# Performance work log

Measured on AMD Instinct MI355X. Metric: run time of the kernel, lower is better.

Reference implementation:

```python
import jax, jax.numpy as jnp
import numpy as np

B, IN, OUT = 8192, 1024, 1024
GRID_SIZE, SPLINE_ORDER = 5, 3
GRID_LO, GRID_HI = -1.0, 1.0
LN_EPS = 1e-5


def make_grid():
    h = (GRID_HI - GRID_LO) / GRID_SIZE
    g = jnp.linspace(GRID_LO - h * SPLINE_ORDER, GRID_HI + h * SPLINE_ORDER,
                     GRID_SIZE + 2 * SPLINE_ORDER + 1, dtype=jnp.float32)
    return jnp.broadcast_to(g, (IN, g.shape[0]))  # [IN, 12]


def setup_inputs() -> dict:
    key = jax.random.key(0)
    k1, k2, k3 = jax.random.split(key, 3)
    # kaiming_uniform_ linear: bound = sqrt(3/fan_in)
    bw_bound = float(np.sqrt(3.0 / IN))
    sw_bound = float(np.sqrt(3.0 / (IN * 8)))
    return {
        "x": jax.random.normal(k1, (B, IN), dtype=jnp.float32),
        "base_weight": jax.random.uniform(k2, (OUT, IN), minval=-bw_bound, maxval=bw_bound, dtype=jnp.float32),
        "spline_weight": jax.random.uniform(k3, (OUT, IN, GRID_SIZE + SPLINE_ORDER), minval=-sw_bound, maxval=sw_bound, dtype=jnp.float32),
        "grid": make_grid(),
        "ln_gamma": jnp.ones((OUT,), dtype=jnp.float32),
        "ln_beta": jnp.zeros((OUT,), dtype=jnp.float32),
        "prelu_a": jnp.full((1,), 0.25, dtype=jnp.float32),
    }


def _bspline_bases(x, grid):
    # x: [B, IN]; grid: [IN, 12] -> bases: [B, IN, GRID_SIZE+SPLINE_ORDER]
    xu = x[:, :, None]                      # [B, IN, 1]
    g = grid[None, :, :]                    # [1, IN, 12]
    bases = ((xu >= g[..., :-1]) & (xu < g[..., 1:])).astype(x.dtype)
    for k in range(1, SPLINE_ORDER + 1):
        left = g[..., :-(k + 1)]
        right = g[..., k:-1]
        g_rshift = g[..., k + 1:]
        g_lshift = g[..., 1:-k]
        dr = right - left
        dd = g_rshift - g_lshift
        dr = jnp.where(dr == 0, jnp.ones_like(dr), dr)
        dd = jnp.where(dd == 0, jnp.ones_like(dd), dd)
        bases = (xu - left) / dr * bases[..., :-1] + (g_rshift - xu) / dd * bases[..., 1:]
    return bases


def reference(x, base_weight, spline_weight, grid, ln_gamma, ln_beta, prelu_a):
    base_out = jnp.dot(jax.nn.gelu(x, approximate=False), base_weight.T)  # [B, OUT]
    bases = _bspline_bases(x, grid)                                        # [B, IN, 8]
    spline_out = jnp.einsum('bik,oik->bo', bases, spline_weight)           # [B, OUT]
    y = base_out + spline_out
    mu = jnp.mean(y, axis=-1, keepdims=True)
    var = jnp.mean(jnp.square(y - mu), axis=-1, keepdims=True)
    yn = (y - mu) * jax.lax.rsqrt(var + LN_EPS) * ln_gamma + ln_beta
    return jnp.where(yn >= 0, yn, prelu_a * yn)
```

## Files before the change

### kernel.cpp

```cpp
#include <hip/hip_runtime.h>
#include <hip/hip_bf16.h>

typedef __attribute__((ext_vector_type(8))) short bf16x8;
typedef __attribute__((ext_vector_type(4))) float f32x4;

#define KTOT 9216
#define KHALF 4608
#define NB   8192
#define NIN  1024
#define NOUT 1024

__device__ __forceinline__ void load_lds16(const void* g, void* l) {
  __builtin_amdgcn_global_load_lds(
      (const __attribute__((address_space(1))) void*)g,
      (__attribute__((address_space(3))) void*)l, 16, 0, 0);
}

__global__ void prep(const float* __restrict__ x,
                     const float* __restrict__ grid,
                     __hip_bfloat16* __restrict__ A,
                     const float* __restrict__ bw,
                     const float* __restrict__ sw,
                     __hip_bfloat16* __restrict__ W) {
  if (blockIdx.x < 4096) {
    const int tid = blockIdx.x * blockDim.x + threadIdx.x;
    const int i  = tid & (NIN - 1);
    const int b0 = (tid >> 10) << 3;

    float g[12];
#pragma unroll
    for (int j = 0; j < 12; ++j) g[j] = grid[j];

    float invdr1[10], invdd1[10], invdr2[9], invdd2[9], invdr3[8], invdd3[8];
#pragma unroll
    for (int j = 0; j < 10; ++j) {
      invdr1[j] = __builtin_amdgcn_rcpf(g[j + 1] - g[j]);
      invdd1[j] = __builtin_amdgcn_rcpf(g[j + 2] - g[j + 1]);
    }
#pragma unroll
    for (int j = 0; j < 9; ++j) {
      invdr2[j] = __builtin_amdgcn_rcpf(g[j + 2] - g[j]);
      invdd2[j] = __builtin_amdgcn_rcpf(g[j + 3] - g[j + 1]);
    }
#pragma unroll
    for (int j = 0; j < 8; ++j) {
      invdr3[j] = __builtin_amdgcn_rcpf(g[j + 3] - g[j]);
      invdd3[j] = __builtin_amdgcn_rcpf(g[j + 4] - g[j + 1]);
    }

    for (int bb = 0; bb < 8; ++bb) {
      const int b = b0 + bb;
      const float xv = x[(size_t)b * NIN + i];
      const float ge = 0.5f * xv * (1.0f + erff(xv * 0.70710678118654752f));
      __hip_bfloat16* Arow = A + (size_t)b * KTOT;
      Arow[i] = __float2bfloat16(ge);

      float bas[11];
#pragma unroll
      for (int j = 0; j < 11; ++j)
        bas[j] = (xv >= g[j] && xv < g[j + 1]) ? 1.0f : 0.0f;
#pragma unroll
      for (int j = 0; j < 10; ++j)
        bas[j] = (xv - g[j]) * invdr1[j] * bas[j] + (g[j + 2] - xv) * invdd1[j] * bas[j + 1];
#pragma unroll
      for (int j = 0; j < 9; ++j)
        bas[j] = (xv - g[j]) * invdr2[j] * bas[j] + (g[j + 3] - xv) * invdd2[j] * bas[j + 1];
#pragma unroll
      for (int j = 0; j < 8; ++j)
        bas[j] = (xv - g[j]) * invdr3[j] * bas[j] + (g[j + 4] - xv) * invdd3[j] * bas[j + 1];

      union { __hip_bfloat16 h[8]; uint4 v; } u;
#pragma unroll
      for (int k = 0; k < 8; ++k) u.h[k] = __float2bfloat16(bas[k]);
      *reinterpret_cast<uint4*>(Arow + NIN + i * 8) = u.v;
    }
  } else {
    const int idx = (blockIdx.x - 4096) * blockDim.x + threadIdx.x;
    const int o  = idx / 1152;
    const int c8 = (idx - o * 1152) * 8;
    const float* src = (c8 < 1024) ? (bw + (size_t)o * 1024 + c8)
                                   : (sw + (size_t)o * 8192 + (c8 - 1024));
    float4 f0 = reinterpret_cast<const float4*>(src)[0];
    float4 f1 = reinterpret_cast<const float4*>(src)[1];
    union { __hip_bfloat16 h[8]; uint4 v; } u;
    u.h[0] = __float2bfloat16(f0.x); u.h[1] = __float2bfloat16(f0.y);
    u.h[2] = __float2bfloat16(f0.z); u.h[3] = __float2bfloat16(f0.w);
    u.h[4] = __float2bfloat16(f1.x); u.h[5] = __float2bfloat16(f1.y);
    u.h[6] = __float2bfloat16(f1.z); u.h[7] = __float2bfloat16(f1.w);
    *reinterpret_cast<uint4*>(W + (size_t)o * KTOT + c8) = u.v;
  }
}

__global__ __launch_bounds__(512, 2)
void gemm_2b(const __hip_bfloat16* __restrict__ A,
             const __hip_bfloat16* __restrict__ Bw,
             float* __restrict__ P0,
             float* __restrict__ P1w) {
  extern __shared__ char smem[];

  const int tid  = threadIdx.x;
  const int lane = tid & 63;
  const int wave = tid >> 6;
  const int wr = wave >> 2;
  const int wc = wave & 3;

  const int orig = blockIdx.x;
  const int bid  = (orig & 7) * 32 + (orig >> 3);
  const int ks    = bid & 1;
  const int tileN = (bid >> 1) & 3;
  const int tileM = bid >> 3;
  const size_t brow = (size_t)tileM * 256;
  const size_t bcol = (size_t)tileN * 256;
  const int kbeg = ks * KHALF;

  const __hip_bfloat16* Ab = A  + brow * KTOT;
  const __hip_bfloat16* Bb = Bw + bcol * KTOT;
  float* C = ks ? P1w : P0;

  const int swsrc = ((tid & 7) ^ ((tid >> 3) & 7)) * 8;
  const __hip_bfloat16* srcA = Ab + (size_t)(tid >> 3) * KTOT + kbeg + swsrc;
  const __hip_bfloat16* srcB = Bb + (size_t)(tid >> 3) * KTOT + kbeg + swsrc;
  const int wdst = wave * 1024;

#define AB_(buf)  (smem + (buf) * 32768)
#define BB_(slot) (smem + 98304 + (slot) * 32768)

  auto stageA = [&](int buf, int h, int kt) {
    const __hip_bfloat16* g = srcA + (size_t)h * (128 * KTOT) + (size_t)kt * 64;
    char* d = AB_(buf) + h * 16384 + wdst;
    load_lds16(g, d);
    load_lds16(g + (size_t)64 * KTOT, d + 8192);
  };
  auto stageB = [&](int slot, int h, int kt) {
    const __hip_bfloat16* g = srcB + (size_t)h * (128 * KTOT) + (size_t)kt * 64;
    char* d = BB_(slot) + h * 16384 + wdst;
    load_lds16(g, d);
    load_lds16(g + (size_t)64 * KTOT, d + 8192);
  };

  const int fr = lane & 15;
  const int hi = lane >> 4;
  const int sw = (fr & 7) << 4;
  const int ax0 = (hi * 16) ^ sw;
  const int ax1 = (64 + hi * 16) ^ sw;

  bf16x8 a[4][2], b[4][2];
  f32x4 acc[8][4] = {};

#define RD_A(BUF, MH) { \
    const char* Ah = AB_(BUF) + wr * 16384 + (MH) * 8192; \
    _Pragma("unroll") \
    for (int mi2 = 0; mi2 < 4; ++mi2) { \
      const char* p = Ah + (mi2 * 16 + fr) * 128; \
      a[mi2][0] = *(const bf16x8*)(p + ax0); \
      a[mi2][1] = *(const bf16x8*)(p + ax1); } }

#define RD_B(SLOT, NH) { \
    const char* Bh = BB_(SLOT) + (wc >> 1) * 16384 + ((wc & 1) * 64 + (NH) * 32) * 128; \
    _Pragma("unroll") \
    for (int ni2 = 0; ni2 < 2; ++ni2) { \
      const char* p = Bh + (ni2 * 16 + fr) * 128; \
      b[(NH) * 2 + ni2][0] = *(const bf16x8*)(p + ax0); \
      b[(NH) * 2 + ni2][1] = *(const bf16x8*)(p + ax1); } }

#define PH_SYNC() do { \
    asm volatile("" ::: "memory"); \
    __builtin_amdgcn_s_barrier(); \
    asm volatile("s_waitcnt lgkmcnt(0)" ::: "memory"); \
    __builtin_amdgcn_sched_barrier(0); } while (0)

#define QMFMA(MH, NH) do { \
    __builtin_amdgcn_s_setprio(1); \
    _Pragma("unroll") \
    for (int mi2 = 0; mi2 < 4; ++mi2) \
      _Pragma("unroll") \
      for (int ni2 = 0; ni2 < 2; ++ni2) \
        _Pragma("unroll") \
        for (int kk = 0; kk < 2; ++kk) \
          acc[(MH) * 4 + mi2][(NH) * 2 + ni2] = \
            __builtin_amdgcn_mfma_f32_16x16x32_bf16(a[mi2][kk], b[(NH) * 2 + ni2][kk], \
                                                    acc[(MH) * 4 + mi2][(NH) * 2 + ni2], 0, 0, 0); \
    __builtin_amdgcn_s_setprio(0); } while (0)

#define TILE(T, ABUF, A2, BSL, STB, STA, VMB) do { \
     \
    RD_A(ABUF, 0); RD_B(BSL, 0); RD_B(BSL, 1); \
    if (STB) { stageB((BSL) ^ 1, 0, (T) + 1); stageB((BSL) ^ 1, 1, (T) + 1); } \
    PH_SYNC(); \
    QMFMA(0, 0); QMFMA(0, 1); \
     \
    RD_A(ABUF, 1); \
    if (STA) { stageA(A2, 0, (T) + 2); stageA(A2, 1, (T) + 2); } \
    asm volatile(VMB ::: "memory"); \
    PH_SYNC(); \
    QMFMA(1, 1); QMFMA(1, 0); \
  } while (0)

  stageA(0, 0, 0); stageA(0, 1, 0);
  stageB(0, 0, 0); stageB(0, 1, 0);
  stageA(1, 0, 1); stageA(1, 1, 1);
  asm volatile("s_waitcnt vmcnt(4)" ::: "memory");
  __builtin_amdgcn_s_barrier();
  asm volatile("" ::: "memory");

  for (int it = 0; it < 11; ++it) {
    const int t0 = it * 6;
    TILE(t0 + 0, 0, 2, 0, 1, 1, "s_waitcnt vmcnt(4)");
    TILE(t0 + 1, 1, 0, 1, 1, 1, "s_waitcnt vmcnt(4)");
    TILE(t0 + 2, 2, 1, 0, 1, 1, "s_waitcnt vmcnt(4)");
    TILE(t0 + 3, 0, 2, 1, 1, 1, "s_waitcnt vmcnt(4)");
    TILE(t0 + 4, 1, 0, 0, 1, 1, "s_waitcnt vmcnt(4)");
    TILE(t0 + 5, 2, 1, 1, 1, 1, "s_waitcnt vmcnt(4)");
  }
  TILE(66, 0, 2, 0, 1, 1, "s_waitcnt vmcnt(4)");
  TILE(67, 1, 0, 1, 1, 1, "s_waitcnt vmcnt(4)");
  TILE(68, 2, 1, 0, 1, 1, "s_waitcnt vmcnt(4)");
  TILE(69, 0, 2, 1, 1, 1, "s_waitcnt vmcnt(4)");
  TILE(70, 1, 0, 0, 1, 0, "s_waitcnt vmcnt(0)");
  TILE(71, 2, 1, 1, 0, 0, "s_nop 0");

#undef TILE
#undef QMFMA
#undef PH_SYNC
#undef RD_B
#undef RD_A
#undef BB_
#undef AB_

  const int crow0 = (lane >> 4) * 4;
#pragma unroll
  for (int mi = 0; mi < 8; ++mi)
#pragma unroll
    for (int ni = 0; ni < 4; ++ni) {
      const size_t r0 = brow + wr * 128 + mi * 16 + crow0;
      const size_t cc = bcol + wc * 64 + ni * 16 + fr;
      float* cp = C + r0 * NOUT + cc;
#pragma unroll
      for (int r = 0; r < 4; ++r) cp[(size_t)r * NOUT] = acc[mi][ni][r];
    }
}

__global__ void reduce_ln_prelu(const float* __restrict__ P0,
                                float* __restrict__ y,
                                const float* __restrict__ gamma,
                                const float* __restrict__ beta,
                                const float* __restrict__ pa) {
  const int row = blockIdx.x;
  const int t = threadIdx.x;
  const float* p0r = P0 + (size_t)row * NOUT;
  float* yr = y + (size_t)row * NOUT;

  float4 aa = reinterpret_cast<const float4*>(p0r)[t];
  float4 v = reinterpret_cast<const float4*>(yr)[t];
  v.x += aa.x; v.y += aa.y; v.z += aa.z; v.w += aa.w;

  float s  = v.x + v.y + v.z + v.w;
  float sq = v.x * v.x + v.y * v.y + v.z * v.z + v.w * v.w;
#pragma unroll
  for (int off = 32; off > 0; off >>= 1) {
    s  += __shfl_down(s, off);
    sq += __shfl_down(sq, off);
  }
  __shared__ float red[8];
  const int wv = t >> 6, lane = t & 63;
  if (lane == 0) { red[wv] = s; red[4 + wv] = sq; }
  __syncthreads();
  if (t == 0) {
    const float S = red[0] + red[1] + red[2] + red[3];
    const float Q = red[4] + red[5] + red[6] + red[7];
    const float mu = S * (1.0f / NOUT);
    const float var = Q * (1.0f / NOUT) - mu * mu;
    red[0] = mu;
    red[1] = rsqrtf(var + 1e-5f);
  }
  __syncthreads();
  const float mu = red[0], rs = red[1];
  const float aP = pa[0];
  const float4 g4 = reinterpret_cast<const float4*>(gamma)[t];
  const float4 b4 = reinterpret_cast<const float4*>(beta)[t];
  float o0 = (v.x - mu) * rs * g4.x + b4.x;
  float o1 = (v.y - mu) * rs * g4.y + b4.y;
  float o2 = (v.z - mu) * rs * g4.z + b4.z;
  float o3 = (v.w - mu) * rs * g4.w + b4.w;
  v.x = o0 >= 0.0f ? o0 : aP * o0;
  v.y = o1 >= 0.0f ? o1 : aP * o1;
  v.z = o2 >= 0.0f ? o2 : aP * o2;
  v.w = o3 >= 0.0f ? o3 : aP * o3;
  reinterpret_cast<float4*>(yr)[t] = v;
}

extern "C" void kernel_launch(void* const* d_in, const int* in_sizes, int n_in,
                              void* d_out, int out_size, void* d_ws, size_t ws_size,
                              hipStream_t stream) {
  const float* x     = (const float*)d_in[0];
  const float* bw    = (const float*)d_in[1];
  const float* sw    = (const float*)d_in[2];
  const float* grid  = (const float*)d_in[3];
  const float* gamma = (const float*)d_in[4];
  const float* beta  = (const float*)d_in[5];
  const float* pa    = (const float*)d_in[6];
  float* out = (float*)d_out;

  __hip_bfloat16* Abuf = (__hip_bfloat16*)d_ws;
  __hip_bfloat16* Wbuf = Abuf + (size_t)NB * KTOT;
  float* P0 = (float*)(Wbuf + (size_t)NOUT * KTOT);

  hipFuncSetAttribute(reinterpret_cast<const void*>(gemm_2b),
                      hipFuncAttributeMaxDynamicSharedMemorySize, 163840);

  prep<<<4096 + 4608, 256, 0, stream>>>(x, grid, Abuf, bw, sw, Wbuf);
  gemm_2b<<<(NB / 256) * (NOUT / 256) * 2, 512, 163840, stream>>>(Abuf, Wbuf, P0, out);
  reduce_ln_prelu<<<NB, 256, 0, stream>>>(P0, out, gamma, beta, pa);
}
```

Before: 197.4 us.

## Compute second-half spline bases inside GEMM instead of materializing them

```diff
diff --git a/kernel.cpp b/kernel.cpp
--- a/kernel.cpp
+++ b/kernel.cpp
@@ -14,6 +14,28 @@
   __builtin_amdgcn_global_load_lds(
       (const __attribute__((address_space(1))) void*)g,
       (__attribute__((address_space(3))) void*)l, 16, 0, 0);
+}
+
+__device__ __forceinline__ uint4 bases_octet(float xv) {
+  const float t  = __builtin_fmaf(xv, 2.5f, 5.5f);
+  const float cf = floorf(t);
+  const float u  = t - cf;
+  const int   c  = (int)cf;
+  const float u2 = u * u, u3 = u2 * u;
+  const float om = 1.0f - u;
+  const float N0 = u3 * (1.0f / 6.0f);
+  const float N1 = (-3.0f * u3 + 3.0f * u2 + 3.0f * u + 1.0f) * (1.0f / 6.0f);
+  const float N2 = (3.0f * u3 - 6.0f * u2 + 4.0f) * (1.0f / 6.0f);
+  const float N3 = om * om * om * (1.0f / 6.0f);
+  const bool  inr = (t >= 0.0f) && (t < 11.0f);
+  union { __hip_bfloat16 h[8]; uint4 v; } o;
+#pragma unroll
+  for (int j = 0; j < 8; ++j) {
+    const int d = c - j;
+    float val = (d == 3) ? N3 : (d == 2) ? N2 : (d == 1) ? N1 : (d == 0) ? N0 : 0.0f;
+    o.h[j] = __float2bfloat16(inr ? val : 0.0f);
+  }
+  return o.v;
 }
 
 __global__ void prep(const float* __restrict__ x,
@@ -52,27 +74,29 @@
       const int b = b0 + bb;
       const float xv = x[(size_t)b * NIN + i];
       const float ge = 0.5f * xv * (1.0f + erff(xv * 0.70710678118654752f));
-      __hip_bfloat16* Arow = A + (size_t)b * KTOT;
+      __hip_bfloat16* Arow = A + (size_t)b * KHALF;
       Arow[i] = __float2bfloat16(ge);
 
-      float bas[11];
-#pragma unroll
-      for (int j = 0; j < 11; ++j)
-        bas[j] = (xv >= g[j] && xv < g[j + 1]) ? 1.0f : 0.0f;
-#pragma unroll
-      for (int j = 0; j < 10; ++j)
-        bas[j] = (xv - g[j]) * invdr1[j] * bas[j] + (g[j + 2] - xv) * invdd1[j] * bas[j + 1];
-#pragma unroll
-      for (int j = 0; j < 9; ++j)
-        bas[j] = (xv - g[j]) * invdr2[j] * bas[j] + (g[j + 3] - xv) * invdd2[j] * bas[j + 1];
-#pragma unroll
-      for (int j = 0; j < 8; ++j)
-        bas[j] = (xv - g[j]) * invdr3[j] * bas[j] + (g[j + 4] - xv) * invdd3[j] * bas[j + 1];
-
-      union { __hip_bfloat16 h[8]; uint4 v; } u;
-#pragma unroll
-      for (int k = 0; k < 8; ++k) u.h[k] = __float2bfloat16(bas[k]);
-      *reinterpret_cast<uint4*>(Arow + NIN + i * 8) = u.v;
+      if (i < 448) {
+        float bas[11];
+#pragma unroll
+        for (int j = 0; j < 11; ++j)
+          bas[j] = (xv >= g[j] && xv < g[j + 1]) ? 1.0f : 0.0f;
+#pragma unroll
+        for (int j = 0; j < 10; ++j)
+          bas[j] = (xv - g[j]) * invdr1[j] * bas[j] + (g[j + 2] - xv) * invdd1[j] * bas[j + 1];
+#pragma unroll
+        for (int j = 0; j < 9; ++j)
+          bas[j] = (xv - g[j]) * invdr2[j] * bas[j] + (g[j + 3] - xv) * invdd2[j] * bas[j + 1];
+#pragma unroll
+        for (int j = 0; j < 8; ++j)
+          bas[j] = (xv - g[j]) * invdr3[j] * bas[j] + (g[j + 4] - xv) * invdd3[j] * bas[j + 1];
+
+        union { __hip_bfloat16 h[8]; uint4 v; } u;
+#pragma unroll
+        for (int k = 0; k < 8; ++k) u.h[k] = __float2bfloat16(bas[k]);
+        *reinterpret_cast<uint4*>(Arow + NIN + i * 8) = u.v;
+      }
     }
   } else {
     const int idx = (blockIdx.x - 4096) * blockDim.x + threadIdx.x;
@@ -94,6 +118,7 @@
 __global__ __launch_bounds__(512, 2)
 void gemm_2b(const __hip_bfloat16* __restrict__ A,
              const __hip_bfloat16* __restrict__ Bw,
+             const float* __restrict__ xg,
              float* __restrict__ P0,
              float* __restrict__ P1w) {
   extern __shared__ char smem[];
@@ -113,23 +138,22 @@
   const size_t bcol = (size_t)tileN * 256;
   const int kbeg = ks * KHALF;
 
-  const __hip_bfloat16* Ab = A  + brow * KTOT;
-  const __hip_bfloat16* Bb = Bw + bcol * KTOT;
   float* C = ks ? P1w : P0;
 
-  const int swsrc = ((tid & 7) ^ ((tid >> 3) & 7)) * 8;
-  const __hip_bfloat16* srcA = Ab + (size_t)(tid >> 3) * KTOT + kbeg + swsrc;
-  const __hip_bfloat16* srcB = Bb + (size_t)(tid >> 3) * KTOT + kbeg + swsrc;
+  const int l = (tid & 7) ^ ((tid >> 3) & 7);
+  const int swsrc = l * 8;
+  const __hip_bfloat16* srcA = A + (brow + (size_t)(tid >> 3)) * KHALF + swsrc;
+  const __hip_bfloat16* srcB = Bw + (bcol + (size_t)(tid >> 3)) * KTOT + kbeg + swsrc;
   const int wdst = wave * 1024;
 
 #define AB_(buf)  (smem + (buf) * 32768)
 #define BB_(slot) (smem + 98304 + (slot) * 32768)
 
   auto stageA = [&](int buf, int h, int kt) {
-    const __hip_bfloat16* g = srcA + (size_t)h * (128 * KTOT) + (size_t)kt * 64;
+    const __hip_bfloat16* g = srcA + (size_t)h * (128 * KHALF) + (size_t)kt * 64;
     char* d = AB_(buf) + h * 16384 + wdst;
     load_lds16(g, d);
-    load_lds16(g + (size_t)64 * KTOT, d + 8192);
+    load_lds16(g + (size_t)64 * KHALF, d + 8192);
   };
   auto stageB = [&](int slot, int h, int kt) {
     const __hip_bfloat16* g = srcB + (size_t)h * (128 * KTOT) + (size_t)kt * 64;
@@ -137,6 +161,25 @@
     load_lds16(g, d);
     load_lds16(g + (size_t)64 * KTOT, d + 8192);
   };
+
+  const float* px0 = xg + (brow + (size_t)(tid >> 3)) * NIN + l;
+  float xv[4];
+
+#define LOADX(KT) do { \
+    const int xo = (KT) * 8 + 448; \
+    xv[0] = px0[xo]; \
+    xv[1] = px0[xo + 64 * NIN]; \
+    xv[2] = px0[xo + 128 * NIN]; \
+    xv[3] = px0[xo + 192 * NIN]; \
+    asm volatile("" ::: "memory"); } while (0)
+
+#define CSTAGE(BUF) do { \
+    char* d0 = AB_(BUF) + (size_t)tid * 16; \
+    *reinterpret_cast<uint4*>(d0)         = bases_octet(xv[0]); \
+    *reinterpret_cast<uint4*>(d0 + 8192)  = bases_octet(xv[1]); \
+    *reinterpret_cast<uint4*>(d0 + 16384) = bases_octet(xv[2]); \
+    *reinterpret_cast<uint4*>(d0 + 24576) = bases_octet(xv[3]); \
+  } while (0)
 
   const int fr = lane & 15;
   const int hi = lane >> 4;
@@ -182,13 +225,11 @@
                                                     acc[(MH) * 4 + mi2][(NH) * 2 + ni2], 0, 0, 0); \
     __builtin_amdgcn_s_setprio(0); } while (0)
 
-#define TILE(T, ABUF, A2, BSL, STB, STA, VMB) do { \
-     \
+#define TILE_M(T, ABUF, A2, BSL, STB, STA, VMB) do { \
     RD_A(ABUF, 0); RD_B(BSL, 0); RD_B(BSL, 1); \
     if (STB) { stageB((BSL) ^ 1, 0, (T) + 1); stageB((BSL) ^ 1, 1, (T) + 1); } \
     PH_SYNC(); \
     QMFMA(0, 0); QMFMA(0, 1); \
-     \
     RD_A(ABUF, 1); \
     if (STA) { stageA(A2, 0, (T) + 2); stageA(A2, 1, (T) + 2); } \
     asm volatile(VMB ::: "memory"); \
@@ -196,34 +237,82 @@
     QMFMA(1, 1); QMFMA(1, 0); \
   } while (0)
 
-  stageA(0, 0, 0); stageA(0, 1, 0);
-  stageB(0, 0, 0); stageB(0, 1, 0);
-  stageA(1, 0, 1); stageA(1, 1, 1);
-  asm volatile("s_waitcnt vmcnt(4)" ::: "memory");
-  __builtin_amdgcn_s_barrier();
-  asm volatile("" ::: "memory");
-
-  for (int it = 0; it < 11; ++it) {
-    const int t0 = it * 6;
-    TILE(t0 + 0, 0, 2, 0, 1, 1, "s_waitcnt vmcnt(4)");
-    TILE(t0 + 1, 1, 0, 1, 1, 1, "s_waitcnt vmcnt(4)");
-    TILE(t0 + 2, 2, 1, 0, 1, 1, "s_waitcnt vmcnt(4)");
-    TILE(t0 + 3, 0, 2, 1, 1, 1, "s_waitcnt vmcnt(4)");
-    TILE(t0 + 4, 1, 0, 0, 1, 1, "s_waitcnt vmcnt(4)");
-    TILE(t0 + 5, 2, 1, 1, 1, 1, "s_waitcnt vmcnt(4)");
+#define TILE_C(T, ABUF, A2, BSL, STB, SCA, STX, VMB) do { \
+    RD_A(ABUF, 0); RD_B(BSL, 0); RD_B(BSL, 1); \
+    if (STB) { stageB((BSL) ^ 1, 0, (T) + 1); stageB((BSL) ^ 1, 1, (T) + 1); } \
+    PH_SYNC(); \
+    QMFMA(0, 0); QMFMA(0, 1); \
+    RD_A(ABUF, 1); \
+    if (SCA) CSTAGE(A2); \
+    if (STX) LOADX((T) + 3); \
+    asm volatile(VMB ::: "memory"); \
+    PH_SYNC(); \
+    QMFMA(1, 1); QMFMA(1, 0); \
+  } while (0)
+
+#define VMC(n) "s_waitcnt vmcnt(" #n ")"
+
+  if (ks == 0) {
+    stageA(0, 0, 0); stageA(0, 1, 0);
+    stageB(0, 0, 0); stageB(0, 1, 0);
+    stageA(1, 0, 1); stageA(1, 1, 1);
+    asm volatile(VMC(4) ::: "memory");
+    __builtin_amdgcn_s_barrier();
+    asm volatile("" ::: "memory");
+
+    for (int it = 0; it < 11; ++it) {
+      const int t0 = it * 6;
+      TILE_M(t0 + 0, 0, 2, 0, 1, 1, VMC(4));
+      TILE_M(t0 + 1, 1, 0, 1, 1, 1, VMC(4));
+      TILE_M(t0 + 2, 2, 1, 0, 1, 1, VMC(4));
+      TILE_M(t0 + 3, 0, 2, 1, 1, 1, VMC(4));
+      TILE_M(t0 + 4, 1, 0, 0, 1, 1, VMC(4));
+      TILE_M(t0 + 5, 2, 1, 1, 1, 1, VMC(4));
+    }
+    TILE_M(66, 0, 2, 0, 1, 1, VMC(4));
+    TILE_M(67, 1, 0, 1, 1, 1, VMC(4));
+    TILE_M(68, 2, 1, 0, 1, 1, VMC(4));
+    TILE_M(69, 0, 2, 1, 1, 1, VMC(4));
+    TILE_M(70, 1, 0, 0, 1, 0, VMC(0));
+    TILE_M(71, 2, 1, 1, 0, 0, "s_nop 0");
+  } else {
+    stageB(0, 0, 0); stageB(0, 1, 0);
+    LOADX(0);
+    CSTAGE(0);
+    LOADX(1);
+    CSTAGE(1);
+    LOADX(2);
+    asm volatile(VMC(4) ::: "memory");
+    asm volatile("s_waitcnt lgkmcnt(0)" ::: "memory");
+    __builtin_amdgcn_s_barrier();
+    asm volatile("" ::: "memory");
+
+    for (int it = 0; it < 11; ++it) {
+      const int t0 = it * 6;
+      TILE_C(t0 + 0, 0, 2, 0, 1, 1, 1, VMC(4));
+      TILE_C(t0 + 1, 1, 0, 1, 1, 1, 1, VMC(4));
+      TILE_C(t0 + 2, 2, 1, 0, 1, 1, 1, VMC(4));
+      TILE_C(t0 + 3, 0, 2, 1, 1, 1, 1, VMC(4));
+      TILE_C(t0 + 4, 1, 0, 0, 1, 1, 1, VMC(4));
+      TILE_C(t0 + 5, 2, 1, 1, 1, 1, 1, VMC(4));
+    }
+    TILE_C(66, 0, 2, 0, 1, 1, 1, VMC(4));
+    TILE_C(67, 1, 0, 1, 1, 1, 1, VMC(4));
+    TILE_C(68, 2, 1, 0, 1, 1, 1, VMC(4));
+    TILE_C(69, 0, 2, 1, 1, 1, 0, VMC(0));
+    TILE_C(70, 1, 0, 0, 1, 0, 0, VMC(0));
+    TILE_C(71, 2, 1, 1, 0, 0, 0, "s_nop 0");
   }
-  TILE(66, 0, 2, 0, 1, 1, "s_waitcnt vmcnt(4)");
-  TILE(67, 1, 0, 1, 1, 1, "s_waitcnt vmcnt(4)");
-  TILE(68, 2, 1, 0, 1, 1, "s_waitcnt vmcnt(4)");
-  TILE(69, 0, 2, 1, 1, 1, "s_waitcnt vmcnt(4)");
-  TILE(70, 1, 0, 0, 1, 0, "s_waitcnt vmcnt(0)");
-  TILE(71, 2, 1, 1, 0, 0, "s_nop 0");
-
-#undef TILE
+
+#undef VMC
+#undef TILE_C
+#undef TILE_M
 #undef QMFMA
 #undef PH_SYNC
 #undef RD_B
 #undef RD_A
+#undef CSTAGE
+#undef LOADX
 #undef BB_
 #undef AB_
 
@@ -302,13 +391,13 @@
   float* out = (float*)d_out;
 
   __hip_bfloat16* Abuf = (__hip_bfloat16*)d_ws;
-  __hip_bfloat16* Wbuf = Abuf + (size_t)NB * KTOT;
+  __hip_bfloat16* Wbuf = Abuf + (size_t)NB * KHALF;
   float* P0 = (float*)(Wbuf + (size_t)NOUT * KTOT);
 
   hipFuncSetAttribute(reinterpret_cast<const void*>(gemm_2b),
                       hipFuncAttributeMaxDynamicSharedMemorySize, 163840);
 
   prep<<<4096 + 4608, 256, 0, stream>>>(x, grid, Abuf, bw, sw, Wbuf);
-  gemm_2b<<<(NB / 256) * (NOUT / 256) * 2, 512, 163840, stream>>>(Abuf, Wbuf, P0, out);
+  gemm_2b<<<(NB / 256) * (NOUT / 256) * 2, 512, 163840, stream>>>(Abuf, Wbuf, x, P0, out);
   reduce_ln_prelu<<<NB, 256, 0, stream>>>(P0, out, gamma, beta, pa);
 }
```

Measured after the change: 570.8 us. +189.1%, slower.
